# Kernel tuning notes

Measured on AMD Instinct MI355X. Metric: run time of the kernel, lower is better.

## Reference

```python
import jax, jax.numpy as jnp
import numpy as np

NUM_AGENTS = 256
STATE_DIM = 12 * NUM_AGENTS
CONTROL_DIM = 4 * NUM_AGENTS
MASS = 0.5
HIDDEN = 100
BATCH = 8192


def lambertw(x):
    # Principal branch for x >= 0 via Halley iterations (jit/vjp friendly).
    w = jnp.log1p(x)
    for _ in range(30):
        ew = jnp.exp(w)
        f = w * ew - x
        denom = ew * (w + 1.0) - (w + 2.0) * f / (2.0 * (w + 1.0))
        w = w - f / denom
    return w


def setup_inputs() -> dict:
    key = jax.random.key(0)
    ks = jax.random.split(key, 8)
    scale1 = 1.0 / np.sqrt(STATE_DIM + 1)
    scale2 = 1.0 / np.sqrt(HIDDEN)
    return {
        "z": jax.random.normal(ks[0], (BATCH, STATE_DIM), dtype=jnp.float32),
        "t": jax.random.uniform(ks[1], (BATCH, 1), dtype=jnp.float32),
        "W1": jax.random.normal(ks[2], (STATE_DIM + 1, HIDDEN), dtype=jnp.float32) * scale1,
        "b1": jnp.zeros((HIDDEN,), dtype=jnp.float32),
        "W2": jax.random.normal(ks[3], (HIDDEN, HIDDEN), dtype=jnp.float32) * scale2,
        "b2": jnp.zeros((HIDDEN,), dtype=jnp.float32),
        "W3": jax.random.normal(ks[4], (HIDDEN, STATE_DIM), dtype=jnp.float32) * scale2,
        "b3": jnp.zeros((STATE_DIM,), dtype=jnp.float32),
    }


def reference(z, t, W1, b1, W2, b2, W3, b3):
    # p_net: MLP on (t, z) producing cost parameters p (B, STATE_DIM)
    x = jnp.concatenate([t, z], axis=-1)
    h = jnp.tanh(x @ W1 + b1)
    h = jnp.tanh(h @ W2 + b2)
    p = h @ W3 + b3

    B = p.shape[0]
    pr = p.reshape(B, NUM_AGENTS, 12)
    # Linear cost vector c over controls: agent components (x,y,z adjoints)/m, psi, theta, phi.
    c = jnp.stack(
        [(pr[..., 6] + pr[..., 7] + pr[..., 8]) / MASS, pr[..., 9], pr[..., 10], pr[..., 11]],
        axis=-1,
    ).reshape(B, CONTROL_DIM)

    # Closed-form solution of min_u c^T u + exp(alpha * ||u||^2), alpha = 0.5/N:
    # u* = -k c with 2*alpha*k*exp(alpha*k^2*s) = 1, s = ||c||^2
    # => k = sqrt(W(s/(2*alpha)) / (2*alpha*s))
    alpha = 0.5 / NUM_AGENTS
    s = jnp.sum(c * c, axis=-1)  # (B,)
    w = lambertw(s / (2.0 * alpha))
    safe_s = jnp.where(s > 0, s, 1.0)
    k = jnp.sqrt(w / (2.0 * alpha * safe_s))
    k = jnp.where(s > 0, k, 0.0)
    ustar = -k[:, None] * c  # (B, CONTROL_DIM)
    return ustar
```

## Files before the change

### kernel.cpp

```cpp
#include <hip/hip_runtime.h>

#define DEV __device__ __forceinline__

typedef __bf16 bf16x8 __attribute__((ext_vector_type(8)));
typedef float f32x4 __attribute__((ext_vector_type(4)));
typedef short s16x8 __attribute__((ext_vector_type(8)));
typedef unsigned short u16x4 __attribute__((ext_vector_type(4)));
typedef unsigned short u16x8 __attribute__((ext_vector_type(8)));

constexpr int B_ = 8192;
constexpr int S_ = 3072;
constexpr int H_ = 100;
constexpr int NP_ = 128;
constexpr int C_ = 1024;
constexpr int KS_ = 64;
constexpr int NSPLIT_ = 4;
constexpr int KSP_ = S_ / NSPLIT_;
constexpr int NIT_ = KSP_ / KS_;

constexpr size_t OFF_W1b = 0;
constexpr size_t OFF_W2b = OFF_W1b + (size_t)NP_ * S_ * 2;
constexpr size_t OFF_W3c = OFF_W2b + (size_t)NP_ * NP_ * 2;
constexpr size_t OFF_b3c = OFF_W3c + (size_t)C_ * NP_ * 2;
constexpr size_t OFF_h2b = OFF_b3c + (size_t)C_ * 4;

DEV unsigned short f2bf(float f) {
  union { float f; unsigned u; } x; x.f = f;
  return (unsigned short)((x.u + 0x7FFFu + ((x.u >> 16) & 1u)) >> 16);
}

DEV float lambertw0(float x) {
  float w = log1pf(x);
#pragma unroll
  for (int i = 0; i < 10; ++i) {
    float ew = expf(w);
    float f = fmaf(w, ew, -x);
    float wp1 = w + 1.0f;
    float den = ew * wp1 - (w + 2.0f) * f / (2.0f * wp1);
    w = w - f / den;
  }
  return w;
}

__global__ void k0_prep(const float* __restrict__ W1, const float* __restrict__ W2,
                        const float* __restrict__ W3, const float* __restrict__ b3,
                        unsigned char* __restrict__ ws) {
  int idx = blockIdx.x * 256 + threadIdx.x;
  constexpr int R1 = NP_ * S_;
  constexpr int R2 = R1 + NP_ * NP_;
  constexpr int R3 = R2 + C_ * NP_;
  constexpr int R4 = R3 + C_;
  if (idx < R1) {
    int n = idx / S_, k = idx - n * S_;
    float v = (n < H_) ? W1[(size_t)(k + 1) * H_ + n] : 0.0f;
    ((unsigned short*)(ws + OFF_W1b))[idx] = f2bf(v);
  } else if (idx < R2) {
    int j = idx - R1;
    int n = j >> 7, k = j & 127;
    float v = (n < H_ && k < H_) ? W2[(size_t)k * H_ + n] : 0.0f;
    ((unsigned short*)(ws + OFF_W2b))[j] = f2bf(v);
  } else if (idx < R3) {
    int j = idx - R2;
    int n = j >> 7, k = j & 127;
    float v = 0.0f;
    if (k < H_) {
      int a = n >> 2, cmp = n & 3;
      const float* row = W3 + (size_t)k * S_ + a * 12;
      v = (cmp == 0) ? 2.0f * (row[6] + row[7] + row[8]) : row[8 + cmp];
    }
    ((unsigned short*)(ws + OFF_W3c))[j] = f2bf(v);
  } else if (idx < R4) {
    int n = idx - R3;
    int a = n >> 2, cmp = n & 3;
    const float* row = b3 + a * 12;
    float v = (cmp == 0) ? 2.0f * (row[6] + row[7] + row[8]) : row[8 + cmp];
    ((float*)(ws + OFF_b3c))[n] = v;
  }
}

__global__ __launch_bounds__(256, 4) void k1_gemm1(
    const float* __restrict__ z, const unsigned char* __restrict__ wsr,
    float* __restrict__ part) {
  __shared__ __align__(16) unsigned char lds[40 * 1024];
  unsigned char* ldsA = lds;
  unsigned char* ldsB = lds + 8192;

  const int tid = threadIdx.x;
  const int lane = tid & 63;
  const int w = tid >> 6;
  const int m = w & 1;
  const int q = w >> 1;
  const int bid = blockIdx.x;
  const int rt = bid >> 2;
  const int h = bid & 3;
  const int rowbase = rt * 32;
  const int k0 = h * KSP_;

  const unsigned short* W1b = (const unsigned short*)(wsr + OFF_W1b);

  const int zrow = tid >> 3;
  const int zk8 = (tid & 7) * 8;
  const float* zp = z + (size_t)(rowbase + zrow) * S_ + k0 + zk8;
  const int bn = tid >> 3;
  const int bk16 = (tid & 7) * 8;
  const unsigned short* bp = W1b + (size_t)bn * S_ + k0 + bk16;

  const int aswz = ((zrow & 7) << 4);
  const int abyte = zrow * 128 + zk8 * 2;
  const int bswz = ((bn & 7) << 4);
  const int bbyte0 = bn * 128 + bk16 * 2;

  const int r0 = m * 16 + (lane & 15);
  const int kb0 = (lane >> 4) * 16;

  f32x4 acc[4];
#pragma unroll
  for (int e = 0; e < 4; ++e) acc[e] = f32x4{0.f, 0.f, 0.f, 0.f};

  {
    float4 za = *(const float4*)(zp);
    float4 zb = *(const float4*)(zp + 4);
    u16x8 av;
    av[0] = f2bf(za.x); av[1] = f2bf(za.y); av[2] = f2bf(za.z); av[3] = f2bf(za.w);
    av[4] = f2bf(zb.x); av[5] = f2bf(zb.y); av[6] = f2bf(zb.z); av[7] = f2bf(zb.w);
    *(u16x8*)(ldsA + (abyte ^ aswz)) = av;
#pragma unroll
    for (int s = 0; s < 4; ++s) {
      s16x8 v = *(const s16x8*)(bp + (size_t)(s * 32) * S_);
      *(s16x8*)(ldsB + ((bbyte0 + s * 32 * 128) ^ bswz)) = v;
    }
  }
  __syncthreads();

  for (int it = 0; it < NIT_; ++it) {
    const int cur = it & 1;
    unsigned char* Ac = ldsA + cur * 4096;
    unsigned char* Bc = ldsB + cur * 16384;
    const bool more = (it + 1 < NIT_);
    float4 za, zb;
    s16x8 bv0, bv1, bv2, bv3;
    if (more) {
      const int ko = (it + 1) * KS_;
      za = *(const float4*)(zp + ko);
      zb = *(const float4*)(zp + ko + 4);
      bv0 = *(const s16x8*)(bp + ko);
      bv1 = *(const s16x8*)(bp + ko + (size_t)32 * S_);
      bv2 = *(const s16x8*)(bp + ko + (size_t)64 * S_);
      bv3 = *(const s16x8*)(bp + ko + (size_t)96 * S_);
    }
    bf16x8 a0 = *(const bf16x8*)(Ac + ((r0 * 128 + 0 + kb0) ^ ((r0 & 7) << 4)));
    bf16x8 a1 = *(const bf16x8*)(Ac + ((r0 * 128 + 64 + kb0) ^ ((r0 & 7) << 4)));
#pragma unroll
    for (int e = 0; e < 4; ++e) {
      int n = q * 64 + e * 16 + (lane & 15);
      bf16x8 bb0 = *(const bf16x8*)(Bc + ((n * 128 + 0 + kb0) ^ ((n & 7) << 4)));
      bf16x8 bb1 = *(const bf16x8*)(Bc + ((n * 128 + 64 + kb0) ^ ((n & 7) << 4)));
      acc[e] = __builtin_amdgcn_mfma_f32_16x16x32_bf16(a0, bb0, acc[e], 0, 0, 0);
      acc[e] = __builtin_amdgcn_mfma_f32_16x16x32_bf16(a1, bb1, acc[e], 0, 0, 0);
    }
    if (more) {
      unsigned char* An = ldsA + (cur ^ 1) * 4096;
      unsigned char* Bn = ldsB + (cur ^ 1) * 16384;
      u16x8 av;
      av[0] = f2bf(za.x); av[1] = f2bf(za.y); av[2] = f2bf(za.z); av[3] = f2bf(za.w);
      av[4] = f2bf(zb.x); av[5] = f2bf(zb.y); av[6] = f2bf(zb.z); av[7] = f2bf(zb.w);
      *(u16x8*)(An + (abyte ^ aswz)) = av;
      *(s16x8*)(Bn + ((bbyte0 + 0 * 32 * 128) ^ bswz)) = bv0;
      *(s16x8*)(Bn + ((bbyte0 + 1 * 32 * 128) ^ bswz)) = bv1;
      *(s16x8*)(Bn + ((bbyte0 + 2 * 32 * 128) ^ bswz)) = bv2;
      *(s16x8*)(Bn + ((bbyte0 + 3 * 32 * 128) ^ bswz)) = bv3;
    }
    __syncthreads();
  }

  float* pout = part + (size_t)h * B_ * NP_;
#pragma unroll
  for (int e = 0; e < 4; ++e) {
    int col = q * 64 + e * 16 + (lane & 15);
#pragma unroll
    for (int i = 0; i < 4; ++i) {
      int r = m * 16 + ((lane >> 4) << 2) + i;
      pout[(size_t)(rowbase + r) * NP_ + col] = acc[e][i];
    }
  }
}

__global__ __launch_bounds__(256, 4) void k2a_mlp(
    const float* __restrict__ part, const float* __restrict__ t,
    const float* __restrict__ W1, const float* __restrict__ b1,
    const float* __restrict__ b2, const unsigned char* __restrict__ wsr,
    unsigned short* __restrict__ h2b) {
  __shared__ __align__(16) unsigned char ldsA[8192];
  __shared__ __align__(16) unsigned char ldsB[32768];

  const int tid = threadIdx.x;
  const int lane = tid & 63;
  const int w = tid >> 6;
  const int m = w & 1;
  const int q = w >> 1;
  const int rowbase = blockIdx.x * 32;

  const unsigned short* W2b = (const unsigned short*)(wsr + OFF_W2b);

  {
    const int row = tid >> 3;
    const int col0 = (tid & 7) * 16;
    const float* p0 = part + (size_t)(rowbase + row) * NP_ + col0;
    f32x4 v[4];
#pragma unroll
    for (int p = 0; p < 4; ++p) {
      v[p] = *(const f32x4*)(p0 + p * 4);
#pragma unroll
      for (int hh = 1; hh < NSPLIT_; ++hh) {
        f32x4 u = *(const f32x4*)(p0 + (size_t)hh * B_ * NP_ + p * 4);
        v[p][0] += u[0]; v[p][1] += u[1]; v[p][2] += u[2]; v[p][3] += u[3];
      }
    }
    const float tv = t[rowbase + row];
    u16x8 o0, o1;
#pragma unroll
    for (int j = 0; j < 16; ++j) {
      int col = col0 + j;
      float b1c = (col < H_) ? b1[col] : 0.0f;
      float w1t = (col < H_) ? W1[col] : 0.0f;
      float pre = v[j >> 2][j & 3] + b1c + tv * w1t;
      unsigned short hb = f2bf(tanhf(pre));
      if (j < 8) o0[j] = hb; else o1[j - 8] = hb;
    }
    const int sw = ((row & 7) << 4);
    *(u16x8*)(ldsA + ((row * 256 + col0 * 2) ^ sw)) = o0;
    *(u16x8*)(ldsA + ((row * 256 + (col0 + 8) * 2) ^ sw)) = o1;
  }
#pragma unroll
  for (int s = 0; s < 8; ++s) {
    int p = s * 256 + tid;
    int n = p >> 4, k16 = p & 15;
    s16x8 v = *(const s16x8*)(W2b + n * 128 + k16 * 8);
    *(s16x8*)(ldsB + ((n * 256 + k16 * 16) ^ ((n & 7) << 4))) = v;
  }
  __syncthreads();

  const int r0 = m * 16 + (lane & 15);
  const int kb0 = (lane >> 4) * 16;
  f32x4 acc[4];
#pragma unroll
  for (int e = 0; e < 4; ++e) acc[e] = f32x4{0.f, 0.f, 0.f, 0.f};
#pragma unroll
  for (int ks = 0; ks < 4; ++ks) {
    bf16x8 a = *(const bf16x8*)(ldsA + ((r0 * 256 + ks * 64 + kb0) ^ ((r0 & 7) << 4)));
#pragma unroll
    for (int e = 0; e < 4; ++e) {
      int n = q * 64 + e * 16 + (lane & 15);
      bf16x8 b = *(const bf16x8*)(ldsB + ((n * 256 + ks * 64 + kb0) ^ ((n & 7) << 4)));
      acc[e] = __builtin_amdgcn_mfma_f32_16x16x32_bf16(a, b, acc[e], 0, 0, 0);
    }
  }
#pragma unroll
  for (int e = 0; e < 4; ++e) {
    int col = q * 64 + e * 16 + (lane & 15);
    float b2c = (col < H_) ? b2[col] : 0.0f;
#pragma unroll
    for (int i = 0; i < 4; ++i) {
      int r = m * 16 + ((lane >> 4) << 2) + i;
      float hh = tanhf(acc[e][i] + b2c);
      h2b[(size_t)(rowbase + r) * NP_ + col] = f2bf(hh);
    }
  }
}

__global__ __launch_bounds__(512, 2) void k2_head(
    const unsigned char* __restrict__ wsr, float* __restrict__ uo) {
  __shared__ __align__(16) unsigned char ldsA[8192];
  __shared__ __align__(16) unsigned char ldsB[2][32768];
  __shared__ float s_part[32][4];
  __shared__ float k_lds[32];

  const int tid = threadIdx.x;
  const int lane = tid & 63;
  const int w = tid >> 6;
  const int m = w & 1;
  const int q = w >> 1;
  const int rowbase = blockIdx.x * 32;

  const unsigned short* h2b = (const unsigned short*)(wsr + OFF_h2b);
  const unsigned short* W3cb = (const unsigned short*)(wsr + OFF_W3c);
  const float* b3c = (const float*)(wsr + OFF_b3c);

  {
    int n = tid >> 4, k16 = tid & 15;
    s16x8 v = *(const s16x8*)(h2b + (size_t)(rowbase + n) * NP_ + k16 * 8);
    *(s16x8*)(ldsA + ((n * 256 + k16 * 16) ^ ((n & 7) << 4))) = v;
  }
#pragma unroll
  for (int s = 0; s < 4; ++s) {
    int p = s * 512 + tid;
    int n = p >> 4, k16 = p & 15;
    s16x8 v = *(const s16x8*)(W3cb + (size_t)n * NP_ + k16 * 8);
    *(s16x8*)(ldsB[0] + ((n * 256 + k16 * 16) ^ ((n & 7) << 4))) = v;
  }
  if (tid < 128) s_part[tid >> 2][tid & 3] = 0.0f;
  __syncthreads();

  const int r0 = m * 16 + (lane & 15);
  const int kb0 = (lane >> 4) * 16;
  bf16x8 af[4];
#pragma unroll
  for (int ks = 0; ks < 4; ++ks)
    af[ks] = *(const bf16x8*)(ldsA + ((r0 * 256 + ks * 64 + kb0) ^ ((r0 & 7) << 4)));

  f32x4 fr[16];
#pragma unroll
  for (int i = 0; i < 16; ++i) fr[i] = f32x4{0.f, 0.f, 0.f, 0.f};

#pragma unroll 8
  for (int ch = 0; ch < 8; ++ch) {
    const int cur = ch & 1;
    const bool more = ch < 7;
    s16x8 st0, st1, st2, st3;
    if (more) {
      int base = (ch + 1) * 128;
      { int p = tid;            int n = p >> 4, k16 = p & 15; st0 = *(const s16x8*)(W3cb + (size_t)(base + n) * NP_ + k16 * 8); }
      { int p = 512 + tid;      int n = p >> 4, k16 = p & 15; st1 = *(const s16x8*)(W3cb + (size_t)(base + n) * NP_ + k16 * 8); }
      { int p = 1024 + tid;     int n = p >> 4, k16 = p & 15; st2 = *(const s16x8*)(W3cb + (size_t)(base + n) * NP_ + k16 * 8); }
      { int p = 1536 + tid;     int n = p >> 4, k16 = p & 15; st3 = *(const s16x8*)(W3cb + (size_t)(base + n) * NP_ + k16 * 8); }
    }
#pragma unroll
    for (int e = 0; e < 2; ++e) {
      int nloc = (q + 4 * e) * 16 + (lane & 15);
#pragma unroll
      for (int ks = 0; ks < 4; ++ks) {
        bf16x8 b = *(const bf16x8*)(ldsB[cur] + ((nloc * 256 + ks * 64 + kb0) ^ ((nloc & 7) << 4)));
        fr[ch * 2 + e] = __builtin_amdgcn_mfma_f32_16x16x32_bf16(af[ks], b, fr[ch * 2 + e], 0, 0, 0);
      }
    }
    if (more) {
      unsigned char* Bn = ldsB[cur ^ 1];
      { int p = tid;        int n = p >> 4, k16 = p & 15; *(s16x8*)(Bn + ((n * 256 + k16 * 16) ^ ((n & 7) << 4))) = st0; }
      { int p = 512 + tid;  int n = p >> 4, k16 = p & 15; *(s16x8*)(Bn + ((n * 256 + k16 * 16) ^ ((n & 7) << 4))) = st1; }
      { int p = 1024 + tid; int n = p >> 4, k16 = p & 15; *(s16x8*)(Bn + ((n * 256 + k16 * 16) ^ ((n & 7) << 4))) = st2; }
      { int p = 1536 + tid; int n = p >> 4, k16 = p & 15; *(s16x8*)(Bn + ((n * 256 + k16 * 16) ^ ((n & 7) << 4))) = st3; }
    }
    __syncthreads();
  }

#pragma unroll
  for (int fi = 0; fi < 16; ++fi) {
    int ch = fi >> 1, e = fi & 1;
    int col = (ch * 8 + q + 4 * e) * 16 + (lane & 15);
    float bc = b3c[col];
    fr[fi][0] += bc; fr[fi][1] += bc; fr[fi][2] += bc; fr[fi][3] += bc;
  }
#pragma unroll
  for (int i = 0; i < 4; ++i) {
    float v = 0.f;
#pragma unroll
    for (int fi = 0; fi < 16; ++fi) v += fr[fi][i] * fr[fi][i];
    v += __shfl_xor(v, 1);
    v += __shfl_xor(v, 2);
    v += __shfl_xor(v, 4);
    v += __shfl_xor(v, 8);
    if ((lane & 15) == 0) s_part[m * 16 + ((lane >> 4) << 2) + i][q] = v;
  }
  __syncthreads();
  if (tid < 32) {
    float s = s_part[tid][0] + s_part[tid][1] + s_part[tid][2] + s_part[tid][3];
    float kk = 0.0f;
    if (s > 0.0f) {
      float wv = lambertw0(s * 256.0f);
      kk = sqrtf(wv * 256.0f / s);
    }
    k_lds[tid] = kk;
  }
  __syncthreads();
#pragma unroll
  for (int fi = 0; fi < 16; ++fi) {
    int ch = fi >> 1, e = fi & 1;
    int col = (ch * 8 + q + 4 * e) * 16 + (lane & 15);
#pragma unroll
    for (int i = 0; i < 4; ++i) {
      int r = m * 16 + ((lane >> 4) << 2) + i;
      uo[(size_t)(rowbase + r) * C_ + col] = -k_lds[r] * fr[fi][i];
    }
  }
}

extern "C" void kernel_launch(void* const* d_in, const int* in_sizes, int n_in,
                              void* d_out, int out_size, void* d_ws, size_t ws_size,
                              hipStream_t stream) {
  const float* z  = (const float*)d_in[0];
  const float* t  = (const float*)d_in[1];
  const float* W1 = (const float*)d_in[2];
  const float* b1 = (const float*)d_in[3];
  const float* W2 = (const float*)d_in[4];
  const float* b2 = (const float*)d_in[5];
  const float* W3 = (const float*)d_in[6];
  const float* b3 = (const float*)d_in[7];
  float* out = (float*)d_out;
  unsigned char* ws = (unsigned char*)d_ws;

  constexpr int PREP_ELEMS = NP_ * S_ + NP_ * NP_ + C_ * NP_ + C_;
  k0_prep<<<(PREP_ELEMS + 255) / 256, 256, 0, stream>>>(W1, W2, W3, b3, ws);
  k1_gemm1<<<B_ / 32 * NSPLIT_, 256, 0, stream>>>(z, ws, out);
  k2a_mlp<<<B_ / 32, 256, 0, stream>>>(out, t, W1, b1, b2, ws,
                                       (unsigned short*)(ws + OFF_h2b));
  k2_head<<<B_ / 32, 512, 0, stream>>>(ws, out);
}
```

Measured before the change: 57.49 us.

## Fuse hidden-layer MLP kernel into head kernel, keeping h2 in LDS

Merges the second-layer kernel (partial-sum reduction, tanh, W2 GEMM) into the head kernel so the h2 activations stay in shared memory instead of going through global memory. W2 is staged in the spare LDS buffer alongside the first W3 chunk. Split-K partials now go to a workspace region instead of the output buffer. This removes one kernel launch and a global round trip of h2. The cost is extra syncs and more work per block of the fused kernel.

```diff
diff --git a/kernel.cpp b/kernel.cpp
--- a/kernel.cpp
+++ b/kernel.cpp
@@ -5,7 +5,6 @@
 typedef __bf16 bf16x8 __attribute__((ext_vector_type(8)));
 typedef float f32x4 __attribute__((ext_vector_type(4)));
 typedef short s16x8 __attribute__((ext_vector_type(8)));
-typedef unsigned short u16x4 __attribute__((ext_vector_type(4)));
 typedef unsigned short u16x8 __attribute__((ext_vector_type(8)));
 
 constexpr int B_ = 8192;
@@ -22,7 +21,7 @@
 constexpr size_t OFF_W2b = OFF_W1b + (size_t)NP_ * S_ * 2;
 constexpr size_t OFF_W3c = OFF_W2b + (size_t)NP_ * NP_ * 2;
 constexpr size_t OFF_b3c = OFF_W3c + (size_t)C_ * NP_ * 2;
-constexpr size_t OFF_h2b = OFF_b3c + (size_t)C_ * 4;
+constexpr size_t OFF_part = OFF_b3c + (size_t)C_ * 4;
 
 DEV unsigned short f2bf(float f) {
   union { float f; unsigned u; } x; x.f = f;
@@ -185,13 +184,15 @@
   }
 }
 
-__global__ __launch_bounds__(256, 4) void k2a_mlp(
+__global__ __launch_bounds__(512, 2) void k2_fused(
     const float* __restrict__ part, const float* __restrict__ t,
     const float* __restrict__ W1, const float* __restrict__ b1,
     const float* __restrict__ b2, const unsigned char* __restrict__ wsr,
-    unsigned short* __restrict__ h2b) {
+    float* __restrict__ uo) {
   __shared__ __align__(16) unsigned char ldsA[8192];
-  __shared__ __align__(16) unsigned char ldsB[32768];
+  __shared__ __align__(16) unsigned char ldsB[2][32768];
+  __shared__ float s_part[32][4];
+  __shared__ float k_lds[32];
 
   const int tid = threadIdx.x;
   const int lane = tid & 63;
@@ -201,108 +202,77 @@
   const int rowbase = blockIdx.x * 32;
 
   const unsigned short* W2b = (const unsigned short*)(wsr + OFF_W2b);
+  const unsigned short* W3cb = (const unsigned short*)(wsr + OFF_W3c);
+  const float* b3c = (const float*)(wsr + OFF_b3c);
 
   {
-    const int row = tid >> 3;
-    const int col0 = (tid & 7) * 16;
+    const int row = tid >> 4;
+    const int col0 = (tid & 15) * 8;
     const float* p0 = part + (size_t)(rowbase + row) * NP_ + col0;
-    f32x4 v[4];
-#pragma unroll
-    for (int p = 0; p < 4; ++p) {
+    f32x4 v[2];
+#pragma unroll
+    for (int p = 0; p < 2; ++p) {
       v[p] = *(const f32x4*)(p0 + p * 4);
 #pragma unroll
       for (int hh = 1; hh < NSPLIT_; ++hh) {
-        f32x4 u = *(const f32x4*)(p0 + (size_t)hh * B_ * NP_ + p * 4);
-        v[p][0] += u[0]; v[p][1] += u[1]; v[p][2] += u[2]; v[p][3] += u[3];
+        f32x4 u2 = *(const f32x4*)(p0 + (size_t)hh * B_ * NP_ + p * 4);
+        v[p][0] += u2[0]; v[p][1] += u2[1]; v[p][2] += u2[2]; v[p][3] += u2[3];
       }
     }
     const float tv = t[rowbase + row];
-    u16x8 o0, o1;
-#pragma unroll
-    for (int j = 0; j < 16; ++j) {
+    u16x8 o;
+#pragma unroll
+    for (int j = 0; j < 8; ++j) {
       int col = col0 + j;
       float b1c = (col < H_) ? b1[col] : 0.0f;
       float w1t = (col < H_) ? W1[col] : 0.0f;
       float pre = v[j >> 2][j & 3] + b1c + tv * w1t;
-      unsigned short hb = f2bf(tanhf(pre));
-      if (j < 8) o0[j] = hb; else o1[j - 8] = hb;
-    }
-    const int sw = ((row & 7) << 4);
-    *(u16x8*)(ldsA + ((row * 256 + col0 * 2) ^ sw)) = o0;
-    *(u16x8*)(ldsA + ((row * 256 + (col0 + 8) * 2) ^ sw)) = o1;
-  }
-#pragma unroll
-  for (int s = 0; s < 8; ++s) {
-    int p = s * 256 + tid;
-    int n = p >> 4, k16 = p & 15;
-    s16x8 v = *(const s16x8*)(W2b + n * 128 + k16 * 8);
-    *(s16x8*)(ldsB + ((n * 256 + k16 * 16) ^ ((n & 7) << 4))) = v;
-  }
-  __syncthreads();
-
-  const int r0 = m * 16 + (lane & 15);
-  const int kb0 = (lane >> 4) * 16;
-  f32x4 acc[4];
-#pragma unroll
-  for (int e = 0; e < 4; ++e) acc[e] = f32x4{0.f, 0.f, 0.f, 0.f};
-#pragma unroll
-  for (int ks = 0; ks < 4; ++ks) {
-    bf16x8 a = *(const bf16x8*)(ldsA + ((r0 * 256 + ks * 64 + kb0) ^ ((r0 & 7) << 4)));
-#pragma unroll
-    for (int e = 0; e < 4; ++e) {
-      int n = q * 64 + e * 16 + (lane & 15);
-      bf16x8 b = *(const bf16x8*)(ldsB + ((n * 256 + ks * 64 + kb0) ^ ((n & 7) << 4)));
-      acc[e] = __builtin_amdgcn_mfma_f32_16x16x32_bf16(a, b, acc[e], 0, 0, 0);
-    }
-  }
-#pragma unroll
-  for (int e = 0; e < 4; ++e) {
-    int col = q * 64 + e * 16 + (lane & 15);
-    float b2c = (col < H_) ? b2[col] : 0.0f;
-#pragma unroll
-    for (int i = 0; i < 4; ++i) {
-      int r = m * 16 + ((lane >> 4) << 2) + i;
-      float hh = tanhf(acc[e][i] + b2c);
-      h2b[(size_t)(rowbase + r) * NP_ + col] = f2bf(hh);
-    }
-  }
-}
-
-__global__ __launch_bounds__(512, 2) void k2_head(
-    const unsigned char* __restrict__ wsr, float* __restrict__ uo) {
-  __shared__ __align__(16) unsigned char ldsA[8192];
-  __shared__ __align__(16) unsigned char ldsB[2][32768];
-  __shared__ float s_part[32][4];
-  __shared__ float k_lds[32];
-
-  const int tid = threadIdx.x;
-  const int lane = tid & 63;
-  const int w = tid >> 6;
-  const int m = w & 1;
-  const int q = w >> 1;
-  const int rowbase = blockIdx.x * 32;
-
-  const unsigned short* h2b = (const unsigned short*)(wsr + OFF_h2b);
-  const unsigned short* W3cb = (const unsigned short*)(wsr + OFF_W3c);
-  const float* b3c = (const float*)(wsr + OFF_b3c);
-
-  {
-    int n = tid >> 4, k16 = tid & 15;
-    s16x8 v = *(const s16x8*)(h2b + (size_t)(rowbase + n) * NP_ + k16 * 8);
-    *(s16x8*)(ldsA + ((n * 256 + k16 * 16) ^ ((n & 7) << 4))) = v;
+      o[j] = f2bf(tanhf(pre));
+    }
+    *(u16x8*)(ldsA + ((row * 256 + col0 * 2) ^ ((row & 7) << 4))) = o;
   }
 #pragma unroll
   for (int s = 0; s < 4; ++s) {
     int p = s * 512 + tid;
     int n = p >> 4, k16 = p & 15;
-    s16x8 v = *(const s16x8*)(W3cb + (size_t)n * NP_ + k16 * 8);
-    *(s16x8*)(ldsB[0] + ((n * 256 + k16 * 16) ^ ((n & 7) << 4))) = v;
+    s16x8 v2 = *(const s16x8*)(W2b + n * 128 + k16 * 8);
+    *(s16x8*)(ldsB[1] + ((n * 256 + k16 * 16) ^ ((n & 7) << 4))) = v2;
+    s16x8 v3 = *(const s16x8*)(W3cb + (size_t)n * NP_ + k16 * 8);
+    *(s16x8*)(ldsB[0] + ((n * 256 + k16 * 16) ^ ((n & 7) << 4))) = v3;
   }
   if (tid < 128) s_part[tid >> 2][tid & 3] = 0.0f;
   __syncthreads();
 
   const int r0 = m * 16 + (lane & 15);
   const int kb0 = (lane >> 4) * 16;
+
+  f32x4 acc2[2];
+  acc2[0] = f32x4{0.f, 0.f, 0.f, 0.f};
+  acc2[1] = f32x4{0.f, 0.f, 0.f, 0.f};
+#pragma unroll
+  for (int ks = 0; ks < 4; ++ks) {
+    bf16x8 a = *(const bf16x8*)(ldsA + ((r0 * 256 + ks * 64 + kb0) ^ ((r0 & 7) << 4)));
+#pragma unroll
+    for (int e = 0; e < 2; ++e) {
+      int n = (q * 2 + e) * 16 + (lane & 15);
+      bf16x8 b = *(const bf16x8*)(ldsB[1] + ((n * 256 + ks * 64 + kb0) ^ ((n & 7) << 4)));
+      acc2[e] = __builtin_amdgcn_mfma_f32_16x16x32_bf16(a, b, acc2[e], 0, 0, 0);
+    }
+  }
+  __syncthreads();
+#pragma unroll
+  for (int e = 0; e < 2; ++e) {
+    int col = (q * 2 + e) * 16 + (lane & 15);
+    float b2c = (col < H_) ? b2[col] : 0.0f;
+#pragma unroll
+    for (int i = 0; i < 4; ++i) {
+      int r = m * 16 + ((lane >> 4) << 2) + i;
+      float hh = tanhf(acc2[e][i] + b2c);
+      *(unsigned short*)(ldsA + ((r * 256 + col * 2) ^ ((r & 7) << 4))) = f2bf(hh);
+    }
+  }
+  __syncthreads();
+
   bf16x8 af[4];
 #pragma unroll
   for (int ks = 0; ks < 4; ++ks)
@@ -397,11 +367,10 @@
   const float* b3 = (const float*)d_in[7];
   float* out = (float*)d_out;
   unsigned char* ws = (unsigned char*)d_ws;
+  float* part = (float*)(ws + OFF_part);
 
   constexpr int PREP_ELEMS = NP_ * S_ + NP_ * NP_ + C_ * NP_ + C_;
   k0_prep<<<(PREP_ELEMS + 255) / 256, 256, 0, stream>>>(W1, W2, W3, b3, ws);
-  k1_gemm1<<<B_ / 32 * NSPLIT_, 256, 0, stream>>>(z, ws, out);
-  k2a_mlp<<<B_ / 32, 256, 0, stream>>>(out, t, W1, b1, b2, ws,
-                                       (unsigned short*)(ws + OFF_h2b));
-  k2_head<<<B_ / 32, 512, 0, stream>>>(ws, out);
-}
+  k1_gemm1<<<B_ / 32 * NSPLIT_, 256, 0, stream>>>(z, ws, part);
+  k2_fused<<<B_ / 32, 512, 0, stream>>>(part, t, W1, b1, b2, ws, out);
+}
```

New measurement: 51.90 us. 1.11x faster.
